# Kernel optimization log

Hardware: AMD Instinct MI355X
Metric: run time of the kernel (lower is better)

## Reference

```python
import jax, jax.numpy as jnp
import numpy as np

B, V, L, D, H, W = 4, 2, 8192, 768, 12, 512  # batch, views, seq, d_model, heads, window


def _layernorm(x, g, b, eps=1e-5):
    # matches torch LayerNorm computed in fp32 then cast back
    x32 = x.astype(jnp.float32)
    m = x32.mean(-1, keepdims=True)
    v = ((x32 - m) ** 2).mean(-1, keepdims=True)
    return ((x32 - m) * jax.lax.rsqrt(v + eps) * g + b).astype(x.dtype)


def _mha(q_in, k_in, v_in, wqkv, bqkv, wo, bo, h):
    # torch nn.MultiheadAttention (eval mode, no mask). inputs [..., S, d]
    d = q_in.shape[-1]
    hd = d // h
    scale = 1.0 / np.sqrt(hd)
    q = (q_in @ wqkv[:d].T + bqkv[:d]).reshape(*q_in.shape[:-1], h, hd)
    k = (k_in @ wqkv[d:2 * d].T + bqkv[d:2 * d]).reshape(*k_in.shape[:-1], h, hd)
    v = (v_in @ wqkv[2 * d:].T + bqkv[2 * d:]).reshape(*v_in.shape[:-1], h, hd)
    scores = jnp.einsum('...qhd,...khd->...hqk', q, k) * scale
    a = jax.nn.softmax(scores, axis=-1)
    o = jnp.einsum('...hqk,...khd->...qhd', a, v).reshape(q_in.shape)
    return o @ wo.T + bo


def reference(x, ln1_g, ln1_b, ln2_g, ln2_b,
              a1_wqkv, a1_bqkv, a1_wo, a1_bo,
              a2_wqkv, a2_bqkv, a2_wo, a2_bo,
              fc_w, fc_b, proj_w, proj_b, index):
    b, v, l, c = x.shape
    y = _layernorm(x, ln1_g, ln1_b)
    shifted = (index % 2 == 1)  # index is a static Python int
    xs = jnp.roll(x, W // 2, axis=2) if shifted else x
    p = l // W
    xw = xs.reshape(b, v, p, W, c)  # window partition (only x is rolled, as in source)
    yw = y.reshape(b, v, p, W, c)
    # cross-view windowed attention: Q=norm view i, K=norm view j, V=raw view i
    v1 = _mha(yw[:, 0], yw[:, 1], xw[:, 0], a1_wqkv, a1_bqkv, a1_wo, a1_bo, H)
    v2 = _mha(yw[:, 1], yw[:, 0], xw[:, 1], a2_wqkv, a2_bqkv, a2_wo, a2_bo, H)
    att = jnp.stack([v1, v2], axis=1).reshape(b, v, l, c)
    if shifted:
        att = jnp.roll(att, -(W // 2), axis=2)
    x = x + att
    y2 = _layernorm(x, ln2_g, ln2_b)
    h = y2 @ fc_w.T + fc_b
    h = h * jax.nn.sigmoid(1.702 * h)  # fast GELU
    return x + (h @ proj_w.T + proj_b)


def setup_inputs() -> dict:
    key = jax.random.key(0)
    ks = jax.random.split(key, 10)
    s = 0.02
    return {
        'x': jax.random.normal(ks[0], (B, V, L, D), jnp.float32),
        'ln1_g': jnp.ones((D,), jnp.float32),
        'ln1_b': jnp.zeros((D,), jnp.float32),
        'ln2_g': jnp.ones((D,), jnp.float32),
        'ln2_b': jnp.zeros((D,), jnp.float32),
        'a1_wqkv': jax.random.normal(ks[1], (3 * D, D), jnp.float32) * s,
        'a1_bqkv': jnp.zeros((3 * D,), jnp.float32),
        'a1_wo': jax.random.normal(ks[2], (D, D), jnp.float32) * s,
        'a1_bo': jnp.zeros((D,), jnp.float32),
        'a2_wqkv': jax.random.normal(ks[3], (3 * D, D), jnp.float32) * s,
        'a2_bqkv': jnp.zeros((3 * D,), jnp.float32),
        'a2_wo': jax.random.normal(ks[4], (D, D), jnp.float32) * s,
        'a2_bo': jnp.zeros((D,), jnp.float32),
        'fc_w': jax.random.normal(ks[5], (4 * D, D), jnp.float32) * s,
        'fc_b': jnp.zeros((4 * D,), jnp.float32),
        'proj_w': jax.random.normal(ks[6], (D, 4 * D), jnp.float32) * s,
        'proj_b': jnp.zeros((D,), jnp.float32),
        'index': 0,
    }
```

## Files before the change

kernel.cpp:

```cpp
#include <hip/hip_runtime.h>
#include <hip/hip_bf16.h>

typedef __bf16 bf16x8 __attribute__((ext_vector_type(8)));
typedef float  f32x4  __attribute__((ext_vector_type(4)));
typedef short  s16x4  __attribute__((ext_vector_type(4)));
typedef unsigned short u16;

#define L2E 1.44269504088896f
#define SBAR  __builtin_amdgcn_s_barrier()
#define SCHED __builtin_amdgcn_sched_barrier(0)

static __device__ __forceinline__ u16 f2bf(float f) {
  unsigned u = __builtin_bit_cast(unsigned, f);
  u += 0x7fffu + ((u >> 16) & 1u);
  return (u16)(u >> 16);
}

static __device__ __forceinline__ void gld_lds16(const void* g, void* l) {
  __builtin_amdgcn_global_load_lds((const __attribute__((address_space(1))) unsigned*)g,
                                   (__attribute__((address_space(3))) unsigned*)l, 16, 0, 0);
}

__global__ __launch_bounds__(256)
void cvtk(const float* __restrict__ s, u16* __restrict__ d, int n) {
  const int i = (blockIdx.x * 256 + threadIdx.x) * 4;
  if (i >= n) return;
  const float4 f = *(const float4*)(s + i);
  s16x4 p;
  p[0] = (short)f2bf(f.x); p[1] = (short)f2bf(f.y);
  p[2] = (short)f2bf(f.z); p[3] = (short)f2bf(f.w);
  *(s16x4*)(d + i) = p;
}

__global__ __launch_bounds__(256)
void lnk(const float* __restrict__ x, const float* __restrict__ gw,
         const float* __restrict__ bw, u16* __restrict__ y,
         u16* __restrict__ xv, int viewmajor) {
  const int lane = threadIdx.x & 63;
  const int tok = blockIdx.x * 4 + (threadIdx.x >> 6);
  const float* xr = x + (size_t)tok * 768;
  float4 v[3];
  float s = 0.f, sq = 0.f;
#pragma unroll
  for (int j = 0; j < 3; ++j) {
    v[j] = *(const float4*)(xr + j * 256 + lane * 4);
    s  += v[j].x + v[j].y + v[j].z + v[j].w;
    sq += v[j].x * v[j].x + v[j].y * v[j].y + v[j].z * v[j].z + v[j].w * v[j].w;
  }
#pragma unroll
  for (int o = 1; o < 64; o <<= 1) { s += __shfl_xor(s, o); sq += __shfl_xor(sq, o); }
  const float mean = s * (1.f / 768.f);
  const float var  = sq * (1.f / 768.f) - mean * mean;
  const float rstd = rsqrtf(var + 1e-5f);
  size_t yrow = (size_t)tok;
  if (viewmajor) {
    const int b_ = tok >> 14, vv = (tok >> 13) & 1, l_ = tok & 8191;
    yrow = ((size_t)((vv << 2) + b_) << 13) + l_;
  }
#pragma unroll
  for (int j = 0; j < 3; ++j) {
    const float4 g4 = *(const float4*)(gw + j * 256 + lane * 4);
    const float4 b4 = *(const float4*)(bw + j * 256 + lane * 4);
    s16x4 py;
    py[0] = (short)f2bf((v[j].x - mean) * rstd * g4.x + b4.x);
    py[1] = (short)f2bf((v[j].y - mean) * rstd * g4.y + b4.y);
    py[2] = (short)f2bf((v[j].z - mean) * rstd * g4.z + b4.z);
    py[3] = (short)f2bf((v[j].w - mean) * rstd * g4.w + b4.w);
    *(s16x4*)(y + yrow * 768 + j * 256 + lane * 4) = py;
    if (xv) {
      s16x4 px;
      px[0] = (short)f2bf(v[j].x); px[1] = (short)f2bf(v[j].y);
      px[2] = (short)f2bf(v[j].z); px[3] = (short)f2bf(v[j].w);
      *(s16x4*)(xv + yrow * 768 + j * 256 + lane * 4) = px;
    }
  }
}

template<int MODE>
__global__ __launch_bounds__(512, 2)
void gemm_bt(const u16* __restrict__ A,
             const u16* __restrict__ B1, const u16* __restrict__ B2,
             const float* __restrict__ b1, const float* __restrict__ b2,
             void* __restrict__ C1, void* __restrict__ C2,
             int N, int K,
             const float* __restrict__ xres, const int* __restrict__ idxp) {
  __shared__ char lds[131072];
  const int t = threadIdx.x;
  const int lane = t & 63;
  const int wid = t >> 6;
  const int wm = wid >> 2, wn = wid & 3;

  const int cpx = gridDim.x >> 3;
  const int bid = (blockIdx.x & 7) * cpx + (blockIdx.x >> 3);
  const int Ntiles = N >> 8;
  const int PPB = Ntiles << 3;
  const int panel = bid / PPB;
  const int rem = bid - panel * PPB;
  const int nt = rem >> 3;
  const int mt = (panel << 3) + (rem & 7);

  const u16* Bsel = B1; const float* bias = b1; int ntl = nt;
  if constexpr (MODE == 5) {
    if (nt >= 3) { Bsel = B2; bias = b2; ntl = nt - 3; }
  } else if constexpr (MODE == 6 || MODE == 7) {
    if (mt >= 128) { Bsel = B2; bias = b2; }
  }

  const int urow = t >> 3;
  const int koff = ((t & 7) ^ (urow & 7)) << 3;
  const u16* Asrc = A + (size_t)(mt * 256 + urow) * K + koff;
  const u16* Bsrc = Bsel + (size_t)(ntl * 256 + urow) * K + koff;
  const int wdst = wid << 10;

  auto stgA = [&](int d, int kt, int u0) {
    char* base = (char*)lds + d * 32768 + wdst;
    gld_lds16(Asrc + (size_t)(u0 * 64) * K + kt * 64, base + u0 * 8192);
    gld_lds16(Asrc + (size_t)(u0 * 64 + 64) * K + kt * 64, base + u0 * 8192 + 8192);
  };
  auto stgB = [&](int d, int kt, int u0) {
    char* base = (char*)lds + 65536 + d * 32768 + wdst;
    gld_lds16(Bsrc + (size_t)(u0 * 64) * K + kt * 64, base + u0 * 8192);
    gld_lds16(Bsrc + (size_t)(u0 * 64 + 64) * K + kt * 64, base + u0 * 8192 + 8192);
  };

  const int c15 = lane & 15, g = lane >> 4;
  const int axor = c15 & 7;
  const char* LAb = (char*)lds + (wm * 128 + c15) * 128;
  const char* LBb = (char*)lds + 65536 + (wn * 64 + c15) * 128;
  bf16x8 av[4][2], bv[4][2];
  auto rdA = [&](int d, int mh) {
#pragma unroll
    for (int m = 0; m < 4; ++m)
#pragma unroll
      for (int ks = 0; ks < 2; ++ks)
        av[m][ks] = *(const bf16x8*)(LAb + d * 32768 + (mh * 64 + m * 16) * 128 +
                                     (((ks << 2) | g) ^ axor) * 16);
  };
  auto rdB = [&](int d) {
#pragma unroll
    for (int n = 0; n < 4; ++n)
#pragma unroll
      for (int ks = 0; ks < 2; ++ks)
        bv[n][ks] = *(const bf16x8*)(LBb + d * 32768 + (n * 16) * 128 +
                                     (((ks << 2) | g) ^ axor) * 16);
  };

  f32x4 acc[8][4] = {};
  auto QD = [&](int mh, int nh) {
    __builtin_amdgcn_s_setprio(1);
#pragma unroll
    for (int ks = 0; ks < 2; ++ks)
#pragma unroll
      for (int m = 0; m < 4; ++m)
#pragma unroll
        for (int n = 0; n < 2; ++n)
          acc[mh * 4 + m][nh * 2 + n] = __builtin_amdgcn_mfma_f32_16x16x32_bf16(
              av[m][ks], bv[nh * 2 + n][ks], acc[mh * 4 + m][nh * 2 + n], 0, 0, 0);
    __builtin_amdgcn_s_setprio(0);
  };

  const int nk = K >> 6, niter = nk >> 1, last = nk - 1;

  stgA(0, 0, 0); stgA(0, 0, 2); stgB(0, 0, 0); stgB(0, 0, 2);
  stgB(1, 1, 0); stgB(1, 1, 2); stgA(1, 1, 0);
  asm volatile("s_waitcnt vmcnt(6)" ::: "memory");
  SBAR;

  for (int it = 0; it < niter; ++it) {
    const int i2 = it * 2;
    const int t1 = (i2 + 1 < nk) ? i2 + 1 : last;
    const int t2 = (i2 + 2 < nk) ? i2 + 2 : last;
    const int t3 = (i2 + 3 < nk) ? i2 + 3 : last;

    rdA(0, 0); rdB(0); stgA(1, t1, 2);
    SCHED; SBAR;
    QD(0, 0);
    stgB(0, t2, 0);
    SCHED; SBAR;
    QD(0, 1);
    rdA(0, 1); stgB(0, t2, 2);
    SCHED; SBAR;
    QD(1, 1);
    stgA(0, t2, 0);
    asm volatile("s_waitcnt vmcnt(6)" ::: "memory");
    SCHED; SBAR;
    QD(1, 0);
    rdA(1, 0); rdB(1); stgA(0, t2, 2);
    SCHED; SBAR;
    QD(0, 0);
    stgB(1, t3, 0);
    SCHED; SBAR;
    QD(0, 1);
    rdA(1, 1); stgB(1, t3, 2);
    SCHED; SBAR;
    QD(1, 1);
    stgA(1, t3, 0);
    asm volatile("s_waitcnt vmcnt(6)" ::: "memory");
    SCHED; SBAR;
    QD(1, 0);
  }

  int shift = 0;
  if constexpr (MODE == 7) shift = (idxp[0] & 1) ? 256 : 0;

  const int rb0 = mt * 256 + wm * 128 + (g << 2);
  const int cb_nt = (MODE == 5) ? ntl : nt;
  const int cbase = cb_nt * 256 + wn * 64 + c15;
#pragma unroll
  for (int mi = 0; mi < 8; ++mi) {
    const int row = rb0 + mi * 16;
#pragma unroll
    for (int nj = 0; nj < 4; ++nj) {
      const int col = cbase + nj * 16;
      const float bvv = bias[col];
      if constexpr (MODE == 3) {
        u16* C = (u16*)C1;
#pragma unroll
        for (int r = 0; r < 4; ++r) {
          const float u = acc[mi][nj][r] + bvv;
          const float e = __builtin_amdgcn_exp2f(-2.45546693f * u);
          C[(size_t)(row + r) * N + col] = f2bf(u / (1.f + e));
        }
      } else if constexpr (MODE == 4) {
        float* C = (float*)C1;
#pragma unroll
        for (int r = 0; r < 4; ++r) {
          const size_t idx = (size_t)(row + r) * 768 + col;
          C[idx] = C[idx] + acc[mi][nj][r] + bvv;
        }
      } else if constexpr (MODE == 5) {
        u16* C = (u16*)(nt >= 3 ? C2 : C1);
#pragma unroll
        for (int r = 0; r < 4; ++r)
          C[(size_t)(row + r) * 768 + col] = f2bf(acc[mi][nj][r] + bvv);
      } else if constexpr (MODE == 6) {
        u16* C = (u16*)(row >= 32768 ? C2 : C1);
        const int r32 = row & 32767;
        const int hh = col >> 6, dd = col & 63;
        const int b_ = r32 >> 13, l_ = r32 & 8191;
        s16x4 pk;
#pragma unroll
        for (int r = 0; r < 4; ++r) pk[r] = (short)f2bf(acc[mi][nj][r] + bvv);
        *(s16x4*)(C + (((size_t)((b_ * 12 + hh) << 6) + dd) << 13) + l_) = pk;
      } else {
        float* C = (float*)C1;
        const int att = row >> 15;
        const int r32 = row & 32767;
        const int b_ = r32 >> 13, p_ = r32 & 8191;
        const int l0 = (p_ - shift) & 8191;
        const size_t rbase = ((size_t)((b_ << 1) + att) << 13) + l0;
#pragma unroll
        for (int r = 0; r < 4; ++r) {
          const size_t idx = (rbase + r) * 768 + col;
          C[idx] = xres[idx] + acc[mi][nj][r] + bvv;
        }
      }
    }
  }
}

__global__ __launch_bounds__(512, 2)
void attnk(const u16* __restrict__ Q1, const u16* __restrict__ K1, const u16* __restrict__ V1,
           const u16* __restrict__ Q2, const u16* __restrict__ K2, const u16* __restrict__ V2,
           u16* __restrict__ O, const int* __restrict__ idxp) {
  __shared__ char lds[131072];
  const int t = threadIdx.x;
  const int lane = t & 63;
  const int c = lane & 15, g = lane >> 4;
  const int wid = t >> 6;
  int bb = blockIdx.x;
  const int h = bb % 12; bb /= 12;
  const int w = bb & 15; bb >>= 4;
  const int b = bb & 3;
  const int a = bb >> 2;
  const int shift = (idxp[0] & 1) ? 256 : 0;

  const u16* Q  = a ? Q2 : Q1;
  const u16* Kb = a ? K2 : K1;
  const u16* Vt = a ? V2 : V1;
  const int kbase = b * 8192 + w * 512;
  const u16* Vts = Vt + ((size_t)(b * 12 + h) << 19);

  const int qrow0 = b * 8192 + w * 512 + wid * 64;
  bf16x8 qf[4][2];
#pragma unroll
  for (int q = 0; q < 4; ++q)
#pragma unroll
    for (int hf = 0; hf < 2; ++hf)
      qf[q][hf] = *(const bf16x8*)(Q + (size_t)(qrow0 + q * 16 + c) * 768 + h * 64 + hf * 32 + g * 8);

  {
    const int r0 = t >> 3, ch = t & 7;
    char* kdst = (char*)lds + (wid << 10);
#pragma unroll
    for (int p = 0; p < 8; ++p) {
      const int row = p * 64 + r0;
      gld_lds16(Kb + (size_t)(kbase + row) * 768 + h * 64 + ((ch ^ (row & 7)) << 3),
                kdst + p * 8192);
    }
    char* vdst = (char*)lds + 65536 + (wid << 10);
#pragma unroll
    for (int p = 0; p < 8; ++p) {
      const int vrow = p * 8 + wid;
      const int cg = lane ^ (vrow & 7);
      const int l = (w * 512 + cg * 8 - shift) & 8191;
      gld_lds16(Vts + (size_t)vrow * 8192 + l, vdst + p * 8192);
    }
  }
  __syncthreads();

  f32x4 oacc[4][4] = {};
  f32x4 psum[4] = {};
  const float CEXP = 0.125f * L2E;
  const char* LK = (char*)lds;
  const char* LV = (char*)lds + 65536;

  auto rdK = [&](int kt, bf16x8& k0, bf16x8& k1) {
    const int krow = kt * 16 + c;
    const int ksw = krow & 7;
    k0 = *(const bf16x8*)(LK + krow * 128 + ((g ^ ksw) << 4));
    k1 = *(const bf16x8*)(LK + krow * 128 + (((4 | g) ^ ksw) << 4));
  };
  auto qk = [&](const bf16x8& k0, const bf16x8& k1, f32x4* sc) {
    const f32x4 z = {0.f, 0.f, 0.f, 0.f};
#pragma unroll
    for (int q = 0; q < 4; ++q) {
      sc[q] = __builtin_amdgcn_mfma_f32_16x16x32_bf16(k0, qf[q][0], z, 0, 0, 0);
      sc[q] = __builtin_amdgcn_mfma_f32_16x16x32_bf16(k1, qf[q][1], sc[q], 0, 0, 0);
    }
  };
  auto rdV = [&](int kt, s16x4* vf) {
#pragma unroll
    for (int df = 0; df < 4; ++df) {
      const int vr = df * 16 + c;
      vf[df] = *(const s16x4*)(LV + vr * 1024 +
                               (((kt * 2 + (g >> 1)) ^ (vr & 7)) << 4) + ((g & 1) << 3));
    }
  };
  auto smx = [&](f32x4* sc, s16x4* pk) {
#pragma unroll
    for (int q = 0; q < 4; ++q) {
      f32x4 pv;
      pv[0] = __builtin_amdgcn_exp2f(sc[q][0] * CEXP);
      pv[1] = __builtin_amdgcn_exp2f(sc[q][1] * CEXP);
      pv[2] = __builtin_amdgcn_exp2f(sc[q][2] * CEXP);
      pv[3] = __builtin_amdgcn_exp2f(sc[q][3] * CEXP);
      psum[q] += pv;
      pk[q][0] = (short)f2bf(pv[0]);
      pk[q][1] = (short)f2bf(pv[1]);
      pk[q][2] = (short)f2bf(pv[2]);
      pk[q][3] = (short)f2bf(pv[3]);
    }
  };
  auto pv16 = [&](s16x4* vf, s16x4* pk) {
#pragma unroll
    for (int df = 0; df < 4; ++df)
#pragma unroll
      for (int q = 0; q < 4; ++q)
        oacc[df][q] = __builtin_amdgcn_mfma_f32_16x16x16bf16_1k(vf[df], pk[q], oacc[df][q], 0, 0, 0);
  };

  bf16x8 k0A, k1A, k0B, k1B;
  f32x4 scA[4], scB[4];
  rdK(0, k0A, k1A);
  qk(k0A, k1A, scA);

#pragma unroll 1
  for (int kt = 0; kt < 32; kt += 2) {
    s16x4 vfc[4], pkc[4];
    rdK(kt + 1, k0B, k1B);
    rdV(kt, vfc);
    qk(k0B, k1B, scB);
    smx(scA, pkc);
    pv16(vfc, pkc);
    if (kt + 2 < 32) { rdK(kt + 2, k0A, k1A); }
    rdV(kt + 1, vfc);
    if (kt + 2 < 32) { qk(k0A, k1A, scA); }
    smx(scB, pkc);
    pv16(vfc, pkc);
  }

  const size_t orow0 = (size_t)(a * 32768 + qrow0);
#pragma unroll
  for (int q = 0; q < 4; ++q) {
    float ss = psum[q][0] + psum[q][1] + psum[q][2] + psum[q][3];
    ss += __shfl_xor(ss, 16);
    ss += __shfl_xor(ss, 32);
    const float inv = 1.f / ss;
#pragma unroll
    for (int df = 0; df < 4; ++df) {
      s16x4 po;
#pragma unroll
      for (int r = 0; r < 4; ++r) po[r] = (short)f2bf(oacc[df][q][r] * inv);
      *(s16x4*)(O + (orow0 + q * 16 + c) * 768 + h * 64 + df * 16 + g * 4) = po;
    }
  }
}

extern "C" void kernel_launch(void* const* d_in, const int* in_sizes, int n_in,
                              void* d_out, int out_size, void* d_ws, size_t ws_size,
                              hipStream_t stream) {
  const float* x       = (const float*)d_in[0];
  const float* ln1_g   = (const float*)d_in[1];
  const float* ln1_b   = (const float*)d_in[2];
  const float* ln2_g   = (const float*)d_in[3];
  const float* ln2_b   = (const float*)d_in[4];
  const float* a1_wqkv = (const float*)d_in[5];
  const float* a1_bqkv = (const float*)d_in[6];
  const float* a1_wo   = (const float*)d_in[7];
  const float* a1_bo   = (const float*)d_in[8];
  const float* a2_wqkv = (const float*)d_in[9];
  const float* a2_bqkv = (const float*)d_in[10];
  const float* a2_wo   = (const float*)d_in[11];
  const float* a2_bo   = (const float*)d_in[12];
  const float* fc_w    = (const float*)d_in[13];
  const float* fc_b    = (const float*)d_in[14];
  const float* proj_w  = (const float*)d_in[15];
  const float* proj_b  = (const float*)d_in[16];
  const int*   idxp    = (const int*)d_in[17];
  float* out = (float*)d_out;

  u16* p = (u16*)d_ws;
  u16* w1  = p; p += (size_t)2304 * 768;
  u16* w2  = p; p += (size_t)2304 * 768;
  u16* wo1 = p; p += (size_t)768 * 768;
  u16* wo2 = p; p += (size_t)768 * 768;
  u16* fcw = p; p += (size_t)3072 * 768;
  u16* pjw = p; p += (size_t)768 * 3072;
  u16* y   = p; p += (size_t)65536 * 768;
  u16* xv  = p; p += (size_t)65536 * 768;
  u16* Q1  = p; p += (size_t)32768 * 768;
  u16* K1  = p; p += (size_t)32768 * 768;
  u16* V1  = p; p += (size_t)32768 * 768;
  u16* Q2  = p; p += (size_t)32768 * 768;
  u16* K2  = p; p += (size_t)32768 * 768;
  u16* V2  = p; p += (size_t)32768 * 768;
  u16* Ob  = p; p += (size_t)65536 * 768;
  u16* hb  = Q1;

  cvtk<<<1728, 256, 0, stream>>>(a1_wqkv, w1, 2304 * 768);
  cvtk<<<1728, 256, 0, stream>>>(a2_wqkv, w2, 2304 * 768);
  cvtk<<<576,  256, 0, stream>>>(a1_wo, wo1, 768 * 768);
  cvtk<<<576,  256, 0, stream>>>(a2_wo, wo2, 768 * 768);
  cvtk<<<2304, 256, 0, stream>>>(fc_w, fcw, 3072 * 768);
  cvtk<<<2304, 256, 0, stream>>>(proj_w, pjw, 768 * 3072);

  lnk<<<16384, 256, 0, stream>>>(x, ln1_g, ln1_b, y, xv, 1);

  const size_t VS = (size_t)32768 * 768;

  gemm_bt<5><<<768, 512, 0, stream>>>(y, w1, w2 + 768 * 768,
                                      a1_bqkv, a2_bqkv + 768,
                                      Q1, K2, 1536, 768, nullptr, idxp);
  gemm_bt<5><<<768, 512, 0, stream>>>(y + VS, w1 + 768 * 768, w2,
                                      a1_bqkv + 768, a2_bqkv,
                                      K1, Q2, 1536, 768, nullptr, idxp);
  gemm_bt<6><<<768, 512, 0, stream>>>(xv, w1 + 2 * 768 * 768, w2 + 2 * 768 * 768,
                                      a1_bqkv + 1536, a2_bqkv + 1536,
                                      V1, V2, 768, 768, nullptr, idxp);

  attnk<<<1536, 512, 0, stream>>>(Q1, K1, V1, Q2, K2, V2, Ob, idxp);

  gemm_bt<7><<<768, 512, 0, stream>>>(Ob, wo1, wo2, a1_bo, a2_bo,
                                      out, nullptr, 768, 768, x, idxp);

  lnk<<<16384, 256, 0, stream>>>(out, ln2_g, ln2_b, y, nullptr, 0);

  gemm_bt<3><<<3072, 512, 0, stream>>>(y, fcw, nullptr, fc_b, nullptr,
                                       hb, nullptr, 3072, 768, nullptr, idxp);

  gemm_bt<4><<<768, 512, 0, stream>>>(hb, pjw, nullptr, proj_b, nullptr,
                                      out, nullptr, 768, 3072, nullptr, idxp);
}
```

Measured before the change: 1.369 ms.

## Replace interleaved GEMM pipeline with simple double-buffered K loop and compile-time shapes

The GEMM's hand-interleaved schedule, which split each K step into eight barrier-separated quarter-tiles with partial vmcnt waits, is replaced by a plain double-buffered loop. Each iteration reads the full A and B fragments, issues the next tile's global-to-LDS loads, runs all MFMAs, then waits on vmcnt(0) and a barrier. N and K become template parameters so address arithmetic and the trip count are constant-folded. The simpler schedule has far fewer barriers but exposes more load latency and raises register pressure from holding both A halves at once.

```diff
diff --git a/kernel.cpp b/kernel.cpp
--- a/kernel.cpp
+++ b/kernel.cpp
@@ -76,13 +76,12 @@
   }
 }
 
-template<int MODE>
+template<int MODE, int NN, int KK>
 __global__ __launch_bounds__(512, 2)
 void gemm_bt(const u16* __restrict__ A,
              const u16* __restrict__ B1, const u16* __restrict__ B2,
              const float* __restrict__ b1, const float* __restrict__ b2,
              void* __restrict__ C1, void* __restrict__ C2,
-             int N, int K,
              const float* __restrict__ xres, const int* __restrict__ idxp) {
   __shared__ char lds[131072];
   const int t = threadIdx.x;
@@ -92,8 +91,8 @@
 
   const int cpx = gridDim.x >> 3;
   const int bid = (blockIdx.x & 7) * cpx + (blockIdx.x >> 3);
-  const int Ntiles = N >> 8;
-  const int PPB = Ntiles << 3;
+  constexpr int Ntiles = NN >> 8;
+  constexpr int PPB = Ntiles << 3;
   const int panel = bid / PPB;
   const int rem = bid - panel * PPB;
   const int nt = rem >> 3;
@@ -108,34 +107,27 @@
 
   const int urow = t >> 3;
   const int koff = ((t & 7) ^ (urow & 7)) << 3;
-  const u16* Asrc = A + (size_t)(mt * 256 + urow) * K + koff;
-  const u16* Bsrc = Bsel + (size_t)(ntl * 256 + urow) * K + koff;
+  const u16* Asrc = A + (size_t)(mt * 256 + urow) * KK + koff;
+  const u16* Bsrc = Bsel + (size_t)(ntl * 256 + urow) * KK + koff;
   const int wdst = wid << 10;
 
   auto stgA = [&](int d, int kt, int u0) {
     char* base = (char*)lds + d * 32768 + wdst;
-    gld_lds16(Asrc + (size_t)(u0 * 64) * K + kt * 64, base + u0 * 8192);
-    gld_lds16(Asrc + (size_t)(u0 * 64 + 64) * K + kt * 64, base + u0 * 8192 + 8192);
+    gld_lds16(Asrc + (size_t)(u0 * 64) * KK + kt * 64, base + u0 * 8192);
+    gld_lds16(Asrc + (size_t)(u0 * 64 + 64) * KK + kt * 64, base + u0 * 8192 + 8192);
   };
   auto stgB = [&](int d, int kt, int u0) {
     char* base = (char*)lds + 65536 + d * 32768 + wdst;
-    gld_lds16(Bsrc + (size_t)(u0 * 64) * K + kt * 64, base + u0 * 8192);
-    gld_lds16(Bsrc + (size_t)(u0 * 64 + 64) * K + kt * 64, base + u0 * 8192 + 8192);
+    gld_lds16(Bsrc + (size_t)(u0 * 64) * KK + kt * 64, base + u0 * 8192);
+    gld_lds16(Bsrc + (size_t)(u0 * 64 + 64) * KK + kt * 64, base + u0 * 8192 + 8192);
   };
 
   const int c15 = lane & 15, g = lane >> 4;
   const int axor = c15 & 7;
   const char* LAb = (char*)lds + (wm * 128 + c15) * 128;
   const char* LBb = (char*)lds + 65536 + (wn * 64 + c15) * 128;
-  bf16x8 av[4][2], bv[4][2];
-  auto rdA = [&](int d, int mh) {
-#pragma unroll
-    for (int m = 0; m < 4; ++m)
-#pragma unroll
-      for (int ks = 0; ks < 2; ++ks)
-        av[m][ks] = *(const bf16x8*)(LAb + d * 32768 + (mh * 64 + m * 16) * 128 +
-                                     (((ks << 2) | g) ^ axor) * 16);
-  };
+
+  bf16x8 bv[4][2], avA[4][2], avB[4][2];
   auto rdB = [&](int d) {
 #pragma unroll
     for (int n = 0; n < 4; ++n)
@@ -144,60 +136,71 @@
         bv[n][ks] = *(const bf16x8*)(LBb + d * 32768 + (n * 16) * 128 +
                                      (((ks << 2) | g) ^ axor) * 16);
   };
+  auto rdA0 = [&](int d) {
+#pragma unroll
+    for (int m = 0; m < 4; ++m)
+#pragma unroll
+      for (int ks = 0; ks < 2; ++ks)
+        avA[m][ks] = *(const bf16x8*)(LAb + d * 32768 + (m * 16) * 128 +
+                                      (((ks << 2) | g) ^ axor) * 16);
+  };
+  auto rdA1 = [&](int d) {
+#pragma unroll
+    for (int m = 0; m < 4; ++m)
+#pragma unroll
+      for (int ks = 0; ks < 2; ++ks)
+        avB[m][ks] = *(const bf16x8*)(LAb + d * 32768 + (64 + m * 16) * 128 +
+                                      (((ks << 2) | g) ^ axor) * 16);
+  };
 
   f32x4 acc[8][4] = {};
-  auto QD = [&](int mh, int nh) {
+  auto QDm0 = [&]() {
     __builtin_amdgcn_s_setprio(1);
 #pragma unroll
     for (int ks = 0; ks < 2; ++ks)
 #pragma unroll
       for (int m = 0; m < 4; ++m)
 #pragma unroll
-        for (int n = 0; n < 2; ++n)
-          acc[mh * 4 + m][nh * 2 + n] = __builtin_amdgcn_mfma_f32_16x16x32_bf16(
-              av[m][ks], bv[nh * 2 + n][ks], acc[mh * 4 + m][nh * 2 + n], 0, 0, 0);
+        for (int n = 0; n < 4; ++n)
+          acc[m][n] = __builtin_amdgcn_mfma_f32_16x16x32_bf16(
+              avA[m][ks], bv[n][ks], acc[m][n], 0, 0, 0);
     __builtin_amdgcn_s_setprio(0);
   };
-
-  const int nk = K >> 6, niter = nk >> 1, last = nk - 1;
+  auto QDm1 = [&]() {
+    __builtin_amdgcn_s_setprio(1);
+#pragma unroll
+    for (int ks = 0; ks < 2; ++ks)
+#pragma unroll
+      for (int m = 0; m < 4; ++m)
+#pragma unroll
+        for (int n = 0; n < 4; ++n)
+          acc[4 + m][n] = __builtin_amdgcn_mfma_f32_16x16x32_bf16(
+              avB[m][ks], bv[n][ks], acc[4 + m][n], 0, 0, 0);
+    __builtin_amdgcn_s_setprio(0);
+  };
+
+  constexpr int nk = KK >> 6;
 
   stgA(0, 0, 0); stgA(0, 0, 2); stgB(0, 0, 0); stgB(0, 0, 2);
-  stgB(1, 1, 0); stgB(1, 1, 2); stgA(1, 1, 0);
-  asm volatile("s_waitcnt vmcnt(6)" ::: "memory");
+  asm volatile("s_waitcnt vmcnt(0)" ::: "memory");
   SBAR;
 
-  for (int it = 0; it < niter; ++it) {
-    const int i2 = it * 2;
-    const int t1 = (i2 + 1 < nk) ? i2 + 1 : last;
-    const int t2 = (i2 + 2 < nk) ? i2 + 2 : last;
-    const int t3 = (i2 + 3 < nk) ? i2 + 3 : last;
-
-    rdA(0, 0); rdB(0); stgA(1, t1, 2);
-    SCHED; SBAR;
-    QD(0, 0);
-    stgB(0, t2, 0);
-    SCHED; SBAR;
-    QD(0, 1);
-    rdA(0, 1); stgB(0, t2, 2);
-    SCHED; SBAR;
-    QD(1, 1);
-    stgA(0, t2, 0);
-    asm volatile("s_waitcnt vmcnt(6)" ::: "memory");
-    SCHED; SBAR;
-    QD(1, 0);
-    rdA(1, 0); rdB(1); stgA(0, t2, 2);
-    SCHED; SBAR;
-    QD(0, 0);
-    stgB(1, t3, 0);
-    SCHED; SBAR;
-    QD(0, 1);
-    rdA(1, 1); stgB(1, t3, 2);
-    SCHED; SBAR;
-    QD(1, 1);
-    stgA(1, t3, 0);
-    asm volatile("s_waitcnt vmcnt(6)" ::: "memory");
-    SCHED; SBAR;
-    QD(1, 0);
+#pragma unroll 1
+  for (int kt = 0; kt < nk; ++kt) {
+    const int d = kt & 1;
+    rdB(d); rdA0(d); rdA1(d);
+    const bool pre = (kt + 1 < nk);
+    if (pre) {
+      stgA(d ^ 1, kt + 1, 0); stgA(d ^ 1, kt + 1, 2);
+      stgB(d ^ 1, kt + 1, 0); stgB(d ^ 1, kt + 1, 2);
+    }
+    SCHED;
+    QDm0();
+    QDm1();
+    if (pre) {
+      asm volatile("s_waitcnt vmcnt(0)" ::: "memory");
+      SCHED; SBAR;
+    }
   }
 
   int shift = 0;
@@ -219,7 +222,7 @@
         for (int r = 0; r < 4; ++r) {
           const float u = acc[mi][nj][r] + bvv;
           const float e = __builtin_amdgcn_exp2f(-2.45546693f * u);
-          C[(size_t)(row + r) * N + col] = f2bf(u / (1.f + e));
+          C[(size_t)(row + r) * NN + col] = f2bf(u / (1.f + e));
         }
       } else if constexpr (MODE == 4) {
         float* C = (float*)C1;
@@ -449,26 +452,26 @@
 
   const size_t VS = (size_t)32768 * 768;
 
-  gemm_bt<5><<<768, 512, 0, stream>>>(y, w1, w2 + 768 * 768,
-                                      a1_bqkv, a2_bqkv + 768,
-                                      Q1, K2, 1536, 768, nullptr, idxp);
-  gemm_bt<5><<<768, 512, 0, stream>>>(y + VS, w1 + 768 * 768, w2,
-                                      a1_bqkv + 768, a2_bqkv,
-                                      K1, Q2, 1536, 768, nullptr, idxp);
-  gemm_bt<6><<<768, 512, 0, stream>>>(xv, w1 + 2 * 768 * 768, w2 + 2 * 768 * 768,
-                                      a1_bqkv + 1536, a2_bqkv + 1536,
-                                      V1, V2, 768, 768, nullptr, idxp);
+  gemm_bt<5, 1536, 768><<<768, 512, 0, stream>>>(y, w1, w2 + 768 * 768,
+                                                 a1_bqkv, a2_bqkv + 768,
+                                                 Q1, K2, nullptr, idxp);
+  gemm_bt<5, 1536, 768><<<768, 512, 0, stream>>>(y + VS, w1 + 768 * 768, w2,
+                                                 a1_bqkv + 768, a2_bqkv,
+                                                 K1, Q2, nullptr, idxp);
+  gemm_bt<6, 768, 768><<<768, 512, 0, stream>>>(xv, w1 + 2 * 768 * 768, w2 + 2 * 768 * 768,
+                                                a1_bqkv + 1536, a2_bqkv + 1536,
+                                                V1, V2, nullptr, idxp);
 
   attnk<<<1536, 512, 0, stream>>>(Q1, K1, V1, Q2, K2, V2, Ob, idxp);
 
-  gemm_bt<7><<<768, 512, 0, stream>>>(Ob, wo1, wo2, a1_bo, a2_bo,
-                                      out, nullptr, 768, 768, x, idxp);
+  gemm_bt<7, 768, 768><<<768, 512, 0, stream>>>(Ob, wo1, wo2, a1_bo, a2_bo,
+                                                out, nullptr, x, idxp);
 
   lnk<<<16384, 256, 0, stream>>>(out, ln2_g, ln2_b, y, nullptr, 0);
 
-  gemm_bt<3><<<3072, 512, 0, stream>>>(y, fcw, nullptr, fc_b, nullptr,
-                                       hb, nullptr, 3072, 768, nullptr, idxp);
-
-  gemm_bt<4><<<768, 512, 0, stream>>>(hb, pjw, nullptr, proj_b, nullptr,
-                                      out, nullptr, 768, 3072, nullptr, idxp);
-}
+  gemm_bt<3, 3072, 768><<<3072, 512, 0, stream>>>(y, fcw, nullptr, fc_b, nullptr,
+                                                  hb, nullptr, nullptr, idxp);
+
+  gemm_bt<4, 768, 3072><<<768, 512, 0, stream>>>(hb, pjw, nullptr, proj_b, nullptr,
+                                                 out, nullptr, nullptr, idxp);
+}
```

After: 1.444 ms. 5.5% more time.
